# Performance work log

Measured on AMD Instinct MI355X. Metric: run time of the kernel, lower is better.

## Reference

```python
import jax, jax.numpy as jnp
import numpy as np

N = 100000   # nodes
E = 800000   # edges (avg degree 8)
D = 384      # feature dim (fixed by GraphConv(384,384))
OUT = 2      # out_channels


def setup_inputs() -> dict:
    key = jax.random.key(0)
    ks = jax.random.split(key, 10)
    s = 1.0 / np.sqrt(D)
    x = jax.random.normal(ks[0], (N, D), jnp.float32)
    edge_index = jax.random.randint(ks[1], (2, E), 0, N, dtype=jnp.int64)
    edge_weight = jax.random.uniform(ks[2], (E,), jnp.float32)
    return {
        "x": x,
        "edge_index": edge_index,
        "edge_weight": edge_weight,
        "W_rel1": jax.random.normal(ks[3], (D, D), jnp.float32) * s,
        "b_rel1": jnp.zeros((D,), jnp.float32),
        "W_root1": jax.random.normal(ks[4], (D, D), jnp.float32) * s,
        "W_rel2": jax.random.normal(ks[5], (D, D), jnp.float32) * s,
        "b_rel2": jnp.zeros((D,), jnp.float32),
        "W_root2": jax.random.normal(ks[6], (D, D), jnp.float32) * s,
        "W_lin": jax.random.normal(ks[7], (D, OUT), jnp.float32) * s,
        "b_lin": jnp.zeros((OUT,), jnp.float32),
    }


def _graph_conv(x, src, dst, ew, W_rel, b_rel, W_root):
    # PyG GraphConv (aggr='mean'): lin_rel(mean_j(ew_j * x_src_j)) + lin_root(x)
    msgs = ew[:, None] * x[src]                                   # [E, D] gather
    agg = jax.ops.segment_sum(msgs, dst, num_segments=N)          # [N, D] scatter
    cnt = jax.ops.segment_sum(jnp.ones_like(ew), dst, num_segments=N)
    mean = agg / jnp.maximum(cnt, 1.0)[:, None]
    return mean @ W_rel + b_rel + x @ W_root


def reference(x, edge_index, edge_weight,
              W_rel1, b_rel1, W_root1,
              W_rel2, b_rel2, W_root2,
              W_lin, b_lin):
    src, dst = edge_index[0], edge_index[1]
    h = jax.nn.relu(_graph_conv(x, src, dst, edge_weight, W_rel1, b_rel1, W_root1))
    # dropout(p=0.3) is identity in eval mode
    y = jax.nn.relu(_graph_conv(h, src, dst, edge_weight, W_rel2, b_rel2, W_root2))
    out = jax.nn.sigmoid(y @ W_lin + b_lin)                        # [N, OUT]
    return (out, y)
```

## Files before the change

### kernel.cpp

```cpp
#include <hip/hip_runtime.h>
#include <hip/hip_bf16.h>

typedef __bf16 bf16_t;
typedef bf16_t bf16x8 __attribute__((ext_vector_type(8)));
typedef float f32x4 __attribute__((ext_vector_type(4)));

typedef __attribute__((address_space(3))) unsigned int lds_u32;
typedef __attribute__((address_space(1))) unsigned int glb_u32;

__device__ __forceinline__ float bflo(unsigned int p){ union{unsigned int u; float f;} c; c.u = p << 16; return c.f; }
__device__ __forceinline__ float bfhi(unsigned int p){ union{unsigned int u; float f;} c; c.u = p & 0xffff0000u; return c.f; }
__device__ __forceinline__ unsigned int f2bfu(float f){
  union{float f; unsigned int u;} c; c.f = f;
  return (c.u + 0x7fffu + ((c.u >> 16) & 1u)) >> 16;
}

__global__ void k_cast_x(const float4* __restrict__ x, uint2* __restrict__ xb, int nq){
  int stride = gridDim.x * blockDim.x;
  for (int i = blockIdx.x * blockDim.x + threadIdx.x; i < nq; i += stride){
    float4 v = x[i];
    uint2 o;
    o.x = f2bfu(v.x) | (f2bfu(v.y) << 16);
    o.y = f2bfu(v.z) | (f2bfu(v.w) << 16);
    xb[i] = o;
  }
}

__global__ void k_castT_w4(const float* __restrict__ W0, const float* __restrict__ W1,
                           const float* __restrict__ W2, const float* __restrict__ W3,
                           unsigned short* __restrict__ T0, unsigned short* __restrict__ T1,
                           unsigned short* __restrict__ T2, unsigned short* __restrict__ T3){
  const float* W; unsigned short* T;
  switch (blockIdx.y){
    case 0: W = W0; T = T0; break;
    case 1: W = W1; T = T1; break;
    case 2: W = W2; T = T2; break;
    default: W = W3; T = T3; break;
  }
  int idx = blockIdx.x * 256 + threadIdx.x;
  int k = idx / 384, n = idx - k * 384;
  T[n * 384 + k] = (unsigned short)f2bfu(W[idx]);
}

__global__ void k_deg(const int* __restrict__ dst, int* __restrict__ deg, int E){
  int stride = gridDim.x * blockDim.x;
  for (int e = blockIdx.x * blockDim.x + threadIdx.x; e < E; e += stride)
    atomicAdd(&deg[dst[e]], 1);
}

__global__ void k_scan1(const int* __restrict__ deg, int* __restrict__ incl,
                        int* __restrict__ bsum, int n){
  __shared__ int wsum[16];
  int t = threadIdx.x, l = t & 63, w = t >> 6;
  int i = blockIdx.x * 1024 + t;
  int v = (i < n) ? deg[i] : 0;
  int xv = v;
  #pragma unroll
  for (int s = 1; s < 64; s <<= 1){
    int y = __shfl_up(xv, s, 64);
    if (l >= s) xv += y;
  }
  if (l == 63) wsum[w] = xv;
  __syncthreads();
  int off = 0;
  for (int k2 = 0; k2 < w; ++k2) off += wsum[k2];
  if (i < n) incl[i] = off + xv;
  if (t == 0){
    int tot = 0;
    for (int k2 = 0; k2 < 16; ++k2) tot += wsum[k2];
    bsum[blockIdx.x] = tot;
  }
}

__global__ void k_scan2(int* __restrict__ bsum, int nb){
  __shared__ int wtot;
  int t = threadIdx.x, l = t & 63, w = t >> 6;
  int v = (t < nb) ? bsum[t] : 0;
  int xv = v;
  #pragma unroll
  for (int s = 1; s < 64; s <<= 1){
    int y = __shfl_up(xv, s, 64);
    if (l >= s) xv += y;
  }
  if (t == 63) wtot = xv;
  __syncthreads();
  int off = (w == 1) ? wtot : 0;
  if (t < nb) bsum[t] = off + xv - v;
}

__global__ void k_scan3(const int* __restrict__ incl, const int* __restrict__ bsum,
                        const int* __restrict__ deg, int* __restrict__ rowptr,
                        int* __restrict__ cursor, int n){
  int i = blockIdx.x * 256 + threadIdx.x;
  if (i < n){
    int r = incl[i] + bsum[i >> 10];
    rowptr[i + 1] = r;
    cursor[i] = r - deg[i];
  }
  if (i == 0) rowptr[0] = 0;
}

__global__ void k_fill(const int* __restrict__ src, const int* __restrict__ dst, const float* __restrict__ ew,
                       int* __restrict__ cursor, int2* __restrict__ csr, int E){
  int stride = gridDim.x * blockDim.x;
  for (int e = blockIdx.x * blockDim.x + threadIdx.x; e < E; e += stride){
    int d = dst[e];
    int pos = atomicAdd(&cursor[d], 1);
    int2 c; c.x = src[e]; c.y = __float_as_int(ew[e]);
    csr[pos] = c;
  }
}

__global__ __launch_bounds__(256) void k_gemm_dual(
    const unsigned short* __restrict__ A, const unsigned short* __restrict__ B1,
    const unsigned short* __restrict__ B2,
    unsigned short* __restrict__ P, unsigned short* __restrict__ R,
    int NN, int q, int r)
{
  __shared__ __align__(16) unsigned short lds[2 * 128 * 32 * 2];
  int t = threadIdx.x, w = t >> 6, l = t & 63;

  int lin = blockIdx.x, xcd = lin & 7, idx = lin >> 3;
  int nl = idx + ((xcd < r) ? xcd * (q + 1) : r * (q + 1) + (xcd - r) * q);
  int mt = nl / 3, nt = nl - mt * 3;
  int m0 = mt * 128, n0 = nt * 128;
  int wrow = (w & 1) * 64, wcol = (w >> 1) * 64;
  int colb = l & 15, kq = l >> 4;

  f32x4 accP[4][4] = {}, accR[4][4] = {};

  int gchunk = (l & 3) ^ ((l >> 3) & 3);

  const unsigned short* pB2[4];
  #pragma unroll
  for (int ni = 0; ni < 4; ++ni)
    pB2[ni] = B2 + (long)(n0 + wcol + ni * 16 + colb) * 384 + kq * 8;

  bf16x8 b2r[2][4];

#define STAGE(buf, kk_) do { \
    int kc_ = (kk_) * 32; \
    _Pragma("unroll") \
    for (int q2 = 0; q2 < 2; ++q2){ \
      int rt = (q2 * 4 + w) * 16 + (l >> 2); \
      int ra = m0 + rt; if (ra >= NN) ra = NN - 1; \
      __builtin_amdgcn_global_load_lds((glb_u32*)(A + (long)ra * 384 + kc_ + gchunk * 8), \
          (lds_u32*)((char*)lds + (buf) * 8192 + (q2 * 4 + w) * 1024), 16, 0, 0); \
      __builtin_amdgcn_global_load_lds((glb_u32*)(B1 + (long)(n0 + rt) * 384 + kc_ + gchunk * 8), \
          (lds_u32*)((char*)lds + 16384 + (buf) * 8192 + (q2 * 4 + w) * 1024), 16, 0, 0); \
    } \
  } while (0)

  STAGE(0, 0);
  #pragma unroll
  for (int ni = 0; ni < 4; ++ni)
    b2r[0][ni] = *(const bf16x8*)(pB2[ni]);
  __syncthreads();

  #pragma unroll
  for (int kk = 0; kk < 12; ++kk){
    const int cur = kk & 1;

    if (kk < 11){
      #pragma unroll
      for (int ni = 0; ni < 4; ++ni)
        b2r[cur ^ 1][ni] = *(const bf16x8*)(pB2[ni] + (kk + 1) * 32);
      STAGE(cur ^ 1, kk + 1);
    }

    const char* bA = (const char*)lds + cur * 8192;
    const char* bB = (const char*)lds + 16384 + cur * 8192;
    bf16x8 af[4], b1f[4];
    #pragma unroll
    for (int mi = 0; mi < 4; ++mi){
      int rA = wrow + mi * 16 + colb;
      af[mi] = *(const bf16x8*)(bA + rA * 64 + ((kq ^ ((rA >> 1) & 3)) << 4));
    }
    #pragma unroll
    for (int ni = 0; ni < 4; ++ni){
      int rB = wcol + ni * 16 + colb;
      b1f[ni] = *(const bf16x8*)(bB + rB * 64 + ((kq ^ ((rB >> 1) & 3)) << 4));
    }
    #pragma unroll
    for (int mi = 0; mi < 4; ++mi)
      #pragma unroll
      for (int ni = 0; ni < 4; ++ni){
        accP[mi][ni] = __builtin_amdgcn_mfma_f32_16x16x32_bf16(af[mi], b1f[ni], accP[mi][ni], 0, 0, 0);
        accR[mi][ni] = __builtin_amdgcn_mfma_f32_16x16x32_bf16(af[mi], b2r[cur][ni], accR[mi][ni], 0, 0, 0);
      }

    __syncthreads();
  }
#undef STAGE

  unsigned short* lr = (unsigned short*)lds;
  #pragma unroll
  for (int pass = 0; pass < 2; ++pass){
    __syncthreads();
    #pragma unroll
    for (int mi = 0; mi < 4; ++mi)
      #pragma unroll
      for (int ni = 0; ni < 4; ++ni){
        f32x4 v = pass ? accR[mi][ni] : accP[mi][ni];
        int col = wcol + ni * 16 + colb;
        #pragma unroll
        for (int rr = 0; rr < 4; ++rr){
          int row = wrow + mi * 16 + kq * 4 + rr;
          lr[row * 128 + col] = (unsigned short)f2bfu(v[rr]);
        }
      }
    __syncthreads();
    unsigned short* O = pass ? R : P;
    #pragma unroll
    for (int p = 0; p < 8; ++p){
      int idx16 = p * 256 + t;
      int row = idx16 >> 4, chunk = idx16 & 15;
      int rg = m0 + row;
      if (rg < NN)
        *(uint4*)(O + (long)rg * 384 + n0 + chunk * 8) =
            *(const uint4*)((const char*)lds + idx16 * 16);
    }
  }
}

template<int FINAL>
__global__ void k_agg2(const unsigned short* __restrict__ Pm, const unsigned short* __restrict__ Rm,
                       const float* __restrict__ bias,
                       const int* __restrict__ rowptr, const int2* __restrict__ csr,
                       unsigned short* __restrict__ hout,
                       float* __restrict__ Y, const float* __restrict__ WL,
                       const float* __restrict__ bl, float* __restrict__ outp,
                       int n_nodes){
  int w = threadIdx.x >> 6, l = threadIdx.x & 63;
  int node = blockIdx.x * 4 + w;
  if (node >= n_nodes) return;
  int e0 = rowptr[node], e1 = rowptr[node + 1];
  float a0=0,a1=0,a2=0,a3=0,a4=0,a5=0;
  const unsigned int* P32 = (const unsigned int*)Pm;
  int e = e0;
  for (; e + 2 <= e1; e += 2){
    int2 c0 = csr[e], c1 = csr[e + 1];
    const unsigned int* x0 = P32 + (long)c0.x * 192;
    const unsigned int* x1 = P32 + (long)c1.x * 192;
    unsigned int p0 = x0[l], p1 = x0[l + 64], p2 = x0[l + 128];
    unsigned int q0 = x1[l], q1 = x1[l + 64], q2 = x1[l + 128];
    float w0 = __int_as_float(c0.y), w1 = __int_as_float(c1.y);
    a0 += w0 * bflo(p0); a1 += w0 * bfhi(p0);
    a2 += w0 * bflo(p1); a3 += w0 * bfhi(p1);
    a4 += w0 * bflo(p2); a5 += w0 * bfhi(p2);
    a0 += w1 * bflo(q0); a1 += w1 * bfhi(q0);
    a2 += w1 * bflo(q1); a3 += w1 * bfhi(q1);
    a4 += w1 * bflo(q2); a5 += w1 * bfhi(q2);
  }
  if (e < e1){
    int2 c0 = csr[e];
    const unsigned int* x0 = P32 + (long)c0.x * 192;
    unsigned int p0 = x0[l], p1 = x0[l + 64], p2 = x0[l + 128];
    float w0 = __int_as_float(c0.y);
    a0 += w0 * bflo(p0); a1 += w0 * bfhi(p0);
    a2 += w0 * bflo(p1); a3 += w0 * bfhi(p1);
    a4 += w0 * bflo(p2); a5 += w0 * bfhi(p2);
  }
  int degn = e1 - e0;
  float inv = 1.0f / (float)(degn > 1 ? degn : 1);

  const unsigned int* R32 = (const unsigned int*)Rm + (long)node * 192;
  unsigned int r0 = R32[l], r1 = R32[l + 64], r2 = R32[l + 128];
  const float2* bias2 = (const float2*)bias;
  float2 b0 = bias2[l], b1 = bias2[l + 64], b2 = bias2[l + 128];

  float h0 = fmaxf(a0 * inv + bflo(r0) + b0.x, 0.0f);
  float h1 = fmaxf(a1 * inv + bfhi(r0) + b0.y, 0.0f);
  float h2 = fmaxf(a2 * inv + bflo(r1) + b1.x, 0.0f);
  float h3 = fmaxf(a3 * inv + bfhi(r1) + b1.y, 0.0f);
  float h4 = fmaxf(a4 * inv + bflo(r2) + b2.x, 0.0f);
  float h5 = fmaxf(a5 * inv + bfhi(r2) + b2.y, 0.0f);

  if (!FINAL){
    unsigned int* O32 = (unsigned int*)hout + (long)node * 192;
    O32[l]       = f2bfu(h0) | (f2bfu(h1) << 16);
    O32[l + 64]  = f2bfu(h2) | (f2bfu(h3) << 16);
    O32[l + 128] = f2bfu(h4) | (f2bfu(h5) << 16);
  } else {
    float2* Y2 = (float2*)Y + (long)node * 192;
    Y2[l]       = make_float2(h0, h1);
    Y2[l + 64]  = make_float2(h2, h3);
    Y2[l + 128] = make_float2(h4, h5);
    const float4* WL4 = (const float4*)WL;
    float4 w0 = WL4[l], w1 = WL4[l + 64], w2 = WL4[l + 128];
    float s0 = h0 * w0.x + h1 * w0.z + h2 * w1.x + h3 * w1.z + h4 * w2.x + h5 * w2.z;
    float s1 = h0 * w0.y + h1 * w0.w + h2 * w1.y + h3 * w1.w + h4 * w2.y + h5 * w2.w;
    #pragma unroll
    for (int m = 32; m; m >>= 1){
      s0 += __shfl_xor(s0, m);
      s1 += __shfl_xor(s1, m);
    }
    if (l == 0){
      outp[(long)node * 2]     = 1.f / (1.f + expf(-(s0 + bl[0])));
      outp[(long)node * 2 + 1] = 1.f / (1.f + expf(-(s1 + bl[1])));
    }
  }
}

extern "C" void kernel_launch(void* const* d_in, const int* in_sizes, int n_in,
                              void* d_out, int out_size, void* d_ws, size_t ws_size,
                              hipStream_t stream) {
  const float* x      = (const float*)d_in[0];
  const int*   ei     = (const int*)d_in[1];
  const float* ew     = (const float*)d_in[2];
  const float* Wrel1  = (const float*)d_in[3];
  const float* brel1  = (const float*)d_in[4];
  const float* Wroot1 = (const float*)d_in[5];
  const float* Wrel2  = (const float*)d_in[6];
  const float* brel2  = (const float*)d_in[7];
  const float* Wroot2 = (const float*)d_in[8];
  const float* Wlin   = (const float*)d_in[9];
  const float* blin   = (const float*)d_in[10];

  const int NN = in_sizes[0] / 384;
  const int E  = in_sizes[2];
  const int* src = ei;
  const int* dst = ei + E;

  char* p = (char*)d_ws;
  auto carve = [&](size_t bytes) -> void* {
    void* r = (void*)p;
    p += (bytes + 255) & ~(size_t)255;
    return r;
  };
  int*   deg     = (int*)carve((size_t)NN * 4);
  int*   rowptr  = (int*)carve((size_t)(NN + 1) * 4);
  int*   cursor  = (int*)carve((size_t)NN * 4);
  int*   incl    = (int*)carve((size_t)NN * 4);
  int*   bsum    = (int*)carve(1024);
  int2*  csr     = (int2*)carve((size_t)E * 8);
  unsigned short* xb = (unsigned short*)carve((size_t)NN * 384 * 2);
  unsigned short* Pb = (unsigned short*)carve((size_t)NN * 384 * 2);
  unsigned short* Rb = (unsigned short*)carve((size_t)NN * 384 * 2);
  unsigned short* WT1 = (unsigned short*)carve(384 * 384 * 2);
  unsigned short* WT2 = (unsigned short*)carve(384 * 384 * 2);
  unsigned short* WT3 = (unsigned short*)carve(384 * 384 * 2);
  unsigned short* WT4 = (unsigned short*)carve(384 * 384 * 2);

  float* out = (float*)d_out;
  float* Y   = out + (size_t)NN * 2;

  int nScanB = (NN + 1023) / 1024;

  hipMemsetAsync(deg, 0, (size_t)NN * 4, stream);
  k_cast_x<<<2048, 256, 0, stream>>>((const float4*)x, (uint2*)xb, NN * 96);
  dim3 wg(576, 4);
  k_castT_w4<<<wg, 256, 0, stream>>>(Wrel1, Wroot1, Wrel2, Wroot2, WT1, WT2, WT3, WT4);
  k_deg<<<1024, 256, 0, stream>>>(dst, deg, E);
  k_scan1<<<nScanB, 1024, 0, stream>>>(deg, incl, bsum, NN);
  k_scan2<<<1, 128, 0, stream>>>(bsum, nScanB);
  k_scan3<<<(NN + 255) / 256, 256, 0, stream>>>(incl, bsum, deg, rowptr, cursor, NN);
  k_fill<<<1024, 256, 0, stream>>>(src, dst, ew, cursor, csr, E);

  int nwg = 3 * ((NN + 127) / 128);
  int q = nwg >> 3, r = nwg & 7;
  int aggBlocks = (NN + 3) / 4;

  k_gemm_dual<<<nwg, 256, 0, stream>>>(xb, WT1, WT2, Pb, Rb, NN, q, r);
  k_agg2<0><<<aggBlocks, 256, 0, stream>>>(Pb, Rb, brel1, rowptr, csr,
                                           xb, nullptr, nullptr, nullptr, nullptr, NN);

  k_gemm_dual<<<nwg, 256, 0, stream>>>(xb, WT3, WT4, Pb, Rb, NN, q, r);
  k_agg2<1><<<aggBlocks, 256, 0, stream>>>(Pb, Rb, brel2, rowptr, csr,
                                           nullptr, Y, Wlin, blin, out, NN);
}
```

Baseline: 649.5 us.

## Give each wave private LDS tiles and drop block barriers in GEMM loop

The dual GEMM now has each wave stage its own 64-row A and B1 slices into a private LDS region. Each wave waits on its own loads with explicit s_waitcnt vmcnt, which removes the per-iteration __syncthreads. The epilogue staging buffer is padded to a 132-element row stride to reduce LDS bank conflicts. In exchange, waves that share rows load them redundantly, so global/L2 traffic rises. LDS per block doubles to 64KB, which may lower occupancy, and the padded rows leave 16-byte epilogue reads at 8-byte-aligned offsets.

```diff
diff --git a/kernel.cpp b/kernel.cpp
--- a/kernel.cpp
+++ b/kernel.cpp
@@ -117,7 +117,7 @@
     unsigned short* __restrict__ P, unsigned short* __restrict__ R,
     int NN, int q, int r)
 {
-  __shared__ __align__(16) unsigned short lds[2 * 128 * 32 * 2];
+  __shared__ __align__(16) unsigned short lds[32768];
   int t = threadIdx.x, w = t >> 6, l = t & 63;
 
   int lin = blockIdx.x, xcd = lin & 7, idx = lin >> 3;
@@ -130,6 +130,7 @@
   f32x4 accP[4][4] = {}, accR[4][4] = {};
 
   int gchunk = (l & 3) ^ ((l >> 3) & 3);
+  char* wbase = (char*)lds + w * 16384;
 
   const unsigned short* pB2[4];
   #pragma unroll
@@ -141,13 +142,13 @@
 #define STAGE(buf, kk_) do { \
     int kc_ = (kk_) * 32; \
     _Pragma("unroll") \
-    for (int q2 = 0; q2 < 2; ++q2){ \
-      int rt = (q2 * 4 + w) * 16 + (l >> 2); \
-      int ra = m0 + rt; if (ra >= NN) ra = NN - 1; \
+    for (int q2 = 0; q2 < 4; ++q2){ \
+      int ra = m0 + wrow + q2 * 16 + (l >> 2); if (ra >= NN) ra = NN - 1; \
       __builtin_amdgcn_global_load_lds((glb_u32*)(A + (long)ra * 384 + kc_ + gchunk * 8), \
-          (lds_u32*)((char*)lds + (buf) * 8192 + (q2 * 4 + w) * 1024), 16, 0, 0); \
-      __builtin_amdgcn_global_load_lds((glb_u32*)(B1 + (long)(n0 + rt) * 384 + kc_ + gchunk * 8), \
-          (lds_u32*)((char*)lds + 16384 + (buf) * 8192 + (q2 * 4 + w) * 1024), 16, 0, 0); \
+          (lds_u32*)(wbase + (buf) * 4096 + q2 * 1024), 16, 0, 0); \
+      int rb = n0 + wcol + q2 * 16 + (l >> 2); \
+      __builtin_amdgcn_global_load_lds((glb_u32*)(B1 + (long)rb * 384 + kc_ + gchunk * 8), \
+          (lds_u32*)(wbase + 8192 + (buf) * 4096 + q2 * 1024), 16, 0, 0); \
     } \
   } while (0)
 
@@ -155,7 +156,6 @@
   #pragma unroll
   for (int ni = 0; ni < 4; ++ni)
     b2r[0][ni] = *(const bf16x8*)(pB2[ni]);
-  __syncthreads();
 
   #pragma unroll
   for (int kk = 0; kk < 12; ++kk){
@@ -166,19 +166,23 @@
       for (int ni = 0; ni < 4; ++ni)
         b2r[cur ^ 1][ni] = *(const bf16x8*)(pB2[ni] + (kk + 1) * 32);
       STAGE(cur ^ 1, kk + 1);
-    }
-
-    const char* bA = (const char*)lds + cur * 8192;
-    const char* bB = (const char*)lds + 16384 + cur * 8192;
+      asm volatile("s_waitcnt vmcnt(12)" ::: "memory");
+    } else {
+      asm volatile("s_waitcnt vmcnt(0)" ::: "memory");
+    }
+    __builtin_amdgcn_sched_barrier(0);
+
+    const char* bA = wbase + cur * 4096;
+    const char* bB = wbase + 8192 + cur * 4096;
     bf16x8 af[4], b1f[4];
     #pragma unroll
     for (int mi = 0; mi < 4; ++mi){
-      int rA = wrow + mi * 16 + colb;
+      int rA = mi * 16 + colb;
       af[mi] = *(const bf16x8*)(bA + rA * 64 + ((kq ^ ((rA >> 1) & 3)) << 4));
     }
     #pragma unroll
     for (int ni = 0; ni < 4; ++ni){
-      int rB = wcol + ni * 16 + colb;
+      int rB = ni * 16 + colb;
       b1f[ni] = *(const bf16x8*)(bB + rB * 64 + ((kq ^ ((rB >> 1) & 3)) << 4));
     }
     #pragma unroll
@@ -188,8 +192,7 @@
         accP[mi][ni] = __builtin_amdgcn_mfma_f32_16x16x32_bf16(af[mi], b1f[ni], accP[mi][ni], 0, 0, 0);
         accR[mi][ni] = __builtin_amdgcn_mfma_f32_16x16x32_bf16(af[mi], b2r[cur][ni], accR[mi][ni], 0, 0, 0);
       }
-
-    __syncthreads();
+    __builtin_amdgcn_sched_barrier(0);
   }
 #undef STAGE
 
@@ -206,7 +209,7 @@
         #pragma unroll
         for (int rr = 0; rr < 4; ++rr){
           int row = wrow + mi * 16 + kq * 4 + rr;
-          lr[row * 128 + col] = (unsigned short)f2bfu(v[rr]);
+          lr[row * 132 + col] = (unsigned short)f2bfu(v[rr]);
         }
       }
     __syncthreads();
@@ -218,7 +221,7 @@
       int rg = m0 + row;
       if (rg < NN)
         *(uint4*)(O + (long)rg * 384 + n0 + chunk * 8) =
-            *(const uint4*)((const char*)lds + idx16 * 16);
+            *(const uint4*)((const char*)lds + row * 264 + chunk * 16);
     }
   }
 }
```

After: 660.6 us. Within noise of the previous version (+1.7%).
